# Performance work log

Hardware: AMD Instinct MI355X
Metric: run time of the kernel (lower is better)

Reference implementation:

```python
import jax, jax.numpy as jnp
import numpy as np

B, S, D = 2, 4096, 512
H = 8
W = 512            # local attention window size
HD = D // H        # head dim
NC = S // W        # number of chunks
HALF = W // 2      # symmetric half-window


def setup_inputs() -> dict:
    key = jax.random.key(0)
    ks = jax.random.split(key, 12)
    s = 1.0 / np.sqrt(D)
    return {
        "val": jax.random.normal(ks[0], (B, S, D), jnp.float32),
        "Wq": jax.random.normal(ks[1], (D, D), jnp.float32) * s,
        "bq": jnp.zeros((D,), jnp.float32),
        "Wk": jax.random.normal(ks[2], (D, D), jnp.float32) * s,
        "bk": jnp.zeros((D,), jnp.float32),
        "Wv": jax.random.normal(ks[3], (D, D), jnp.float32) * s,
        "bv": jnp.zeros((D,), jnp.float32),
        "Wo": jax.random.normal(ks[4], (D, D), jnp.float32) * s,
        "bo": jnp.zeros((D,), jnp.float32),
        "gamma": jnp.ones((D,), jnp.float32),
        "beta": jnp.zeros((D,), jnp.float32),
    }


def _heads(x):
    # [B,S,D] -> [B,H,S,HD]
    return x.reshape(B, S, H, HD).transpose(0, 2, 1, 3)


def _gather_neighbors(x):
    # x: [B,H,S,HD] -> [B,H,NC,3W,HD] (prev | cur | next chunk, zero-padded at ends)
    xp = jnp.pad(x, ((0, 0), (0, 0), (W, W), (0, 0)))
    xc = xp.reshape(B, H, NC + 2, W, HD)
    return jnp.concatenate([xc[:, :, :-2], xc[:, :, 1:-1], xc[:, :, 2:]], axis=3)


def _local_attention(x, Wq, bq, Wk, bk, Wv, bv, Wo, bo):
    q = _heads(x @ Wq + bq)
    k = _heads(x @ Wk + bk)
    v = _heads(x @ Wv + bv)

    qc = q.reshape(B, H, NC, W, HD)            # chunked queries
    kn = _gather_neighbors(k)                  # [B,H,NC,3W,HD]
    vn = _gather_neighbors(v)

    scale = 1.0 / np.sqrt(HD)
    scores = jnp.einsum("bhcqd,bhckd->bhcqk", qc, kn) * scale  # [B,H,NC,W,3W]

    # banded mask: key relative position in [-HALF, HALF], and key index in [0,S)
    qi = jnp.arange(W)[:, None]
    kj = jnp.arange(3 * W)[None, :]
    band = jnp.abs(kj - W - qi) <= HALF                          # [W,3W]
    key_pos = (jnp.arange(NC)[:, None, None] - 1) * W + kj[None]  # [NC,1,3W]
    valid = (key_pos >= 0) & (key_pos < S)                       # [NC,1,3W]
    mask = band[None] & valid                                    # [NC,W,3W]

    scores = jnp.where(mask[None, None], scores, jnp.float32(-1e9))
    p = jax.nn.softmax(scores, axis=-1)
    o = jnp.einsum("bhcqk,bhckd->bhcqd", p, vn)                  # [B,H,NC,W,HD]
    o = o.reshape(B, H, S, HD).transpose(0, 2, 1, 3).reshape(B, S, D)
    return o @ Wo + bo


def _layer_norm(x, gamma, beta, eps=1e-5):
    mu = jnp.mean(x, axis=-1, keepdims=True)
    var = jnp.mean(jnp.square(x - mu), axis=-1, keepdims=True)
    return (x - mu) * jax.lax.rsqrt(var + eps) * gamma + beta


def reference(val, Wq, bq, Wk, bk, Wv, bv, Wo, bo, gamma, beta):
    attn_out = _local_attention(val, Wq, bq, Wk, bk, Wv, bv, Wo, bo)
    return _layer_norm(val + attn_out, gamma, beta)
```

## Files before the change

kernel.cpp:

```cpp
#include <hip/hip_runtime.h>
#include <hip/hip_bf16.h>

#define BATCH 2
#define SEQ   4096
#define DIM   512
#define NHEAD 8
#define HDIM  64
#define ROWS  (BATCH*SEQ)

typedef float  fx4   __attribute__((ext_vector_type(4)));
typedef __bf16 bf16x8 __attribute__((ext_vector_type(8)));
typedef unsigned short ushort_t;
typedef unsigned short usx4 __attribute__((ext_vector_type(4)));
typedef unsigned short usx8 __attribute__((ext_vector_type(8)));

static __device__ __forceinline__ float b2f(ushort_t v) {
    union { unsigned int u; float f; } c; c.u = ((unsigned int)v) << 16; return c.f;
}
static __device__ __forceinline__ ushort_t f2b(float f) {
    union { float f; unsigned int u; } c; c.f = f;
    unsigned int u = c.u;
    unsigned int r = (u + 0x7FFFu + ((u >> 16) & 1u)) >> 16;
    return (ushort_t)r;
}
static __device__ __forceinline__ void gload16(const ushort_t* g, ushort_t* l) {
    __builtin_amdgcn_global_load_lds(
        (const __attribute__((address_space(1))) unsigned int*)g,
        (__attribute__((address_space(3))) unsigned int*)l, 16, 0, 0);
}

__global__ __launch_bounds__(256) void cvt_bf16_kernel(const float* __restrict__ x,
                                                       ushort_t* __restrict__ y, int n) {
    int i = (blockIdx.x * 256 + threadIdx.x) * 4;
    if (i < n) {
        fx4 v = *(const fx4*)(x + i);
        usx4 o; o.x = f2b(v.x); o.y = f2b(v.y); o.z = f2b(v.z); o.w = f2b(v.w);
        *(usx4*)(y + i) = o;
    }
}

__global__ __launch_bounds__(256) void transpose4_bf16_kernel(
    const float* __restrict__ W0, const float* __restrict__ W1,
    const float* __restrict__ W2, const float* __restrict__ W3,
    ushort_t* __restrict__ T0, ushort_t* __restrict__ T1,
    ushort_t* __restrict__ T2, ushort_t* __restrict__ T3) {
    const float* W; ushort_t* WT;
    switch (blockIdx.y) {
        case 0: W = W0; WT = T0; break;
        case 1: W = W1; WT = T1; break;
        case 2: W = W2; WT = T2; break;
        default: W = W3; WT = T3; break;
    }
    __shared__ float tile[64][65];
    int r0 = (blockIdx.x & 7) * 64;
    int c0 = (blockIdx.x >> 3) * 64;
    int tid = threadIdx.x;
    for (int idx = tid; idx < 4096; idx += 256) {
        int rr = idx >> 6, cc = idx & 63;
        tile[rr][cc] = W[(c0 + rr) * 512 + (r0 + cc)];
    }
    __syncthreads();
    for (int idx = tid; idx < 4096; idx += 256) {
        int rr = idx >> 6, cc = idx & 63;
        WT[(size_t)(r0 + rr) * 512 + (c0 + cc)] = f2b(tile[cc][rr]);
    }
}

__global__ __launch_bounds__(256) void gemm128_kernel(
    const ushort_t* __restrict__ A,
    const ushort_t* __restrict__ BT0, const ushort_t* __restrict__ BT1, const ushort_t* __restrict__ BT2,
    const float* __restrict__ b0, const float* __restrict__ b1, const float* __restrict__ b2,
    ushort_t* __restrict__ C0, ushort_t* __restrict__ C1, ushort_t* __restrict__ C2) {

    const ushort_t* BT; const float* bias; ushort_t* C;
    if (blockIdx.z == 0)      { BT = BT0; bias = b0; C = C0; }
    else if (blockIdx.z == 1) { BT = BT1; bias = b1; C = C1; }
    else                      { BT = BT2; bias = b2; C = C2; }

    __shared__ ushort_t As[2][128 * 32];
    __shared__ ushort_t Bs[2][128 * 32];

    const int tid  = threadIdx.x;
    const int wave = tid >> 6;
    const int lane = tid & 63;
    const int lm   = lane & 15;
    const int quad = lane >> 4;
    const int wm   = wave >> 1;
    const int wn   = wave & 1;

    const int m0t = blockIdx.x * 128;
    const int n0t = blockIdx.y * 128;

    const int srow = tid >> 2, sgc = tid & 3;
    const ushort_t* ga0 = A  + (size_t)(m0t + srow) * 512 + sgc * 8;
    const ushort_t* ga1 = A  + (size_t)(m0t + srow + 64) * 512 + sgc * 8;
    const ushort_t* gb0 = BT + (size_t)(n0t + srow) * 512 + sgc * 8;
    const ushort_t* gb1 = BT + (size_t)(n0t + srow + 64) * 512 + sgc * 8;

    const int aoff = (wm * 64 + lm) * 32 + quad * 8;
    const int boff = (wn * 64 + lm) * 32 + quad * 8;

    fx4 acc[4][4];
    #pragma unroll
    for (int i = 0; i < 4; ++i)
        #pragma unroll
        for (int j = 0; j < 4; ++j) acc[i][j] = 0;

    for (int k0 = 0; k0 < 512; k0 += 64) {
        __syncthreads();
        #pragma unroll
        for (int p = 0; p < 2; ++p) {
            gload16(ga0 + k0 + p * 32, &As[p][tid * 8]);
            gload16(ga1 + k0 + p * 32, &As[p][(tid + 256) * 8]);
            gload16(gb0 + k0 + p * 32, &Bs[p][tid * 8]);
            gload16(gb1 + k0 + p * 32, &Bs[p][(tid + 256) * 8]);
        }
        __syncthreads();

        #pragma unroll
        for (int p = 0; p < 2; ++p) {
            bf16x8 af[4], bfr[4];
            #pragma unroll
            for (int ms = 0; ms < 4; ++ms) af[ms]  = *(const bf16x8*)&As[p][aoff + ms * 512];
            #pragma unroll
            for (int ns = 0; ns < 4; ++ns) bfr[ns] = *(const bf16x8*)&Bs[p][boff + ns * 512];
            #pragma unroll
            for (int ms = 0; ms < 4; ++ms)
                #pragma unroll
                for (int ns = 0; ns < 4; ++ns)
                    acc[ms][ns] = __builtin_amdgcn_mfma_f32_16x16x32_bf16(af[ms], bfr[ns], acc[ms][ns], 0, 0, 0);
        }
    }

    const int crow0 = m0t + wm * 64 + quad * 4;
    const int ccol0 = n0t + wn * 64 + lm;

    if (blockIdx.z == 2) {
        #pragma unroll
        for (int ns = 0; ns < 4; ++ns) {
            int col = ccol0 + ns * 16;
            int h = col >> 6, d = col & 63;
            float bv = bias[col];
            #pragma unroll
            for (int ms = 0; ms < 4; ++ms) {
                int m = crow0 + ms * 16;
                int bb = m >> 12, s0 = m & 4095;
                usx4 o;
                o.x = f2b(acc[ms][ns][0] + bv); o.y = f2b(acc[ms][ns][1] + bv);
                o.z = f2b(acc[ms][ns][2] + bv); o.w = f2b(acc[ms][ns][3] + bv);
                *(usx4*)(C + (((size_t)(bb * 8 + h) * 64 + d) * 4096 + s0)) = o;
            }
        }
    } else {
        #pragma unroll
        for (int ns = 0; ns < 4; ++ns) {
            int col = ccol0 + ns * 16;
            float bv = bias[col];
            #pragma unroll
            for (int ms = 0; ms < 4; ++ms) {
                #pragma unroll
                for (int r = 0; r < 4; ++r) {
                    C[(size_t)(crow0 + ms * 16 + r) * 512 + col] = f2b(acc[ms][ns][r] + bv);
                }
            }
        }
    }
}

__global__ __launch_bounds__(256) void attn_mfma_kernel(
    const ushort_t* __restrict__ Qb, const ushort_t* __restrict__ Kb,
    const ushort_t* __restrict__ Vt, ushort_t* __restrict__ Ob) {

    __shared__ ushort_t Klds[64 * 64];
    __shared__ ushort_t Vlds[64 * 64];
    __shared__ ushort_t Plds[4 * 32 * 72];

    const int tid  = threadIdx.x;
    const int wave = tid >> 6;
    const int lane = tid & 63;
    const int lm   = lane & 15;
    const int quad = lane >> 4;

    const int bh = blockIdx.y;
    const int b = bh >> 3, h = bh & 7;
    const int q0 = blockIdx.x * 128;
    const int qw = q0 + wave * 32;

    bf16x8 qf[2][2];
    #pragma unroll
    for (int qs = 0; qs < 2; ++qs) {
        const ushort_t* qp = Qb + ((size_t)(b * SEQ + qw + qs * 16 + lm)) * 512 + h * 64 + quad * 8;
        qf[qs][0] = *(const bf16x8*)qp;
        qf[qs][1] = *(const bf16x8*)(qp + 32);
    }

    int koff[2][4], voff[2][4];
    #pragma unroll
    for (int ks = 0; ks < 2; ++ks) {
        #pragma unroll
        for (int tn = 0; tn < 4; ++tn) {
            int key = tn * 16 + lm;
            koff[ks][tn] = key * 64 + (((ks * 4 + quad) ^ (key & 7)) * 8);
            int d = tn * 16 + lm;
            voff[ks][tn] = d * 64 + (((ks * 4 + quad) ^ (d & 7)) * 8);
        }
    }
    ushort_t* Pw = Plds + wave * (32 * 72);
    int pread[2][2];
    #pragma unroll
    for (int qs = 0; qs < 2; ++qs)
        #pragma unroll
        for (int ks = 0; ks < 2; ++ks)
            pread[qs][ks] = (qs * 16 + lm) * 72 + ks * 32 + quad * 8;

    const int skey = tid >> 3;
    const int sdg  = tid & 7;
    const size_t kgbase = ((size_t)b * SEQ) * 512 + h * 64 + sdg * 8;
    const size_t vgbase = ((size_t)bh * 64) * 4096 + sdg * 8;
    const int l0 = skey * 64 + ((sdg ^ (skey & 7)) * 8);
    const int l1 = l0 + 32 * 64;

    const int klo = (q0 >= 256) ? 0 : ((256 - q0) >> 6);
    const int khi = min(9, (4288 - q0) >> 6);
    const int wlo = wave >> 1, whi = 8 + (wave >> 1);
    const int flo = 1 + (wave >> 1), fhi = 7 + (wave >> 1);

    bf16x8 onesf;
    {
        __bf16 o = (lm == 0) ? (__bf16)1.0f : (__bf16)0.0f;
        #pragma unroll
        for (int j = 0; j < 8; ++j) onesf[j] = o;
    }

    fx4 oacc[2][4];
    #pragma unroll
    for (int qs = 0; qs < 2; ++qs)
        #pragma unroll
        for (int tn = 0; tn < 4; ++tn) oacc[qs][tn] = 0;
    fx4 lacc[2];
    lacc[0] = 0; lacc[1] = 0;

    usx8 kn0, kn1, vn0, vn1;
    {
        int ts = q0 - 256 + klo * 64;
        kn0 = *(const usx8*)(Kb + kgbase + (size_t)(ts + skey) * 512);
        kn1 = *(const usx8*)(Kb + kgbase + (size_t)(ts + skey + 32) * 512);
        vn0 = *(const usx8*)(Vt + vgbase + (size_t)skey * 4096 + ts);
        vn1 = *(const usx8*)(Vt + vgbase + (size_t)(skey + 32) * 4096 + ts);
    }

    for (int kt = klo; kt <= khi; ++kt) {
        const int ts = q0 - 256 + kt * 64;
        __syncthreads();
        *(usx8*)&Klds[l0] = kn0;
        *(usx8*)&Klds[l1] = kn1;
        *(usx8*)&Vlds[l0] = vn0;
        *(usx8*)&Vlds[l1] = vn1;
        __syncthreads();

        if (kt < khi) {
            int t2 = ts + 64;
            kn0 = *(const usx8*)(Kb + kgbase + (size_t)(t2 + skey) * 512);
            kn1 = *(const usx8*)(Kb + kgbase + (size_t)(t2 + skey + 32) * 512);
            vn0 = *(const usx8*)(Vt + vgbase + (size_t)skey * 4096 + t2);
            vn1 = *(const usx8*)(Vt + vgbase + (size_t)(skey + 32) * 4096 + t2);
        }

        if (kt < wlo || kt > whi) continue;

        bf16x8 kf[2][4];
        #pragma unroll
        for (int ks = 0; ks < 2; ++ks)
            #pragma unroll
            for (int tn = 0; tn < 4; ++tn)
                kf[ks][tn] = *(const bf16x8*)&Klds[koff[ks][tn]];
        fx4 sacc[2][4];
        #pragma unroll
        for (int qs = 0; qs < 2; ++qs)
            #pragma unroll
            for (int tn = 0; tn < 4; ++tn) sacc[qs][tn] = 0;
        #pragma unroll
        for (int ks = 0; ks < 2; ++ks)
            #pragma unroll
            for (int tn = 0; tn < 4; ++tn) {
                sacc[0][tn] = __builtin_amdgcn_mfma_f32_16x16x32_bf16(qf[0][ks], kf[ks][tn], sacc[0][tn], 0, 0, 0);
                sacc[1][tn] = __builtin_amdgcn_mfma_f32_16x16x32_bf16(qf[1][ks], kf[ks][tn], sacc[1][tn], 0, 0, 0);
            }

        const bool edge = (kt < flo) || (kt > fhi);
        #pragma unroll
        for (int qs = 0; qs < 2; ++qs) {
            #pragma unroll
            for (int tn = 0; tn < 4; ++tn) {
                int kg = ts + tn * 16 + lm;
                #pragma unroll
                for (int r = 0; r < 4; ++r) {
                    float p = __expf(sacc[qs][tn][r] * 0.125f);
                    if (edge) {
                        int dlt = kg - (qw + qs * 16 + quad * 4 + r);
                        p = (dlt <= 256 && dlt >= -256) ? p : 0.0f;
                    }
                    Pw[(qs * 16 + quad * 4 + r) * 72 + tn * 16 + lm] = f2b(p);
                }
            }
        }

        bf16x8 vf[2][4];
        #pragma unroll
        for (int ks = 0; ks < 2; ++ks)
            #pragma unroll
            for (int tn = 0; tn < 4; ++tn)
                vf[ks][tn] = *(const bf16x8*)&Vlds[voff[ks][tn]];
        #pragma unroll
        for (int qs = 0; qs < 2; ++qs) {
            #pragma unroll
            for (int ks = 0; ks < 2; ++ks) {
                bf16x8 ap = *(const bf16x8*)&Pw[pread[qs][ks]];
                lacc[qs] = __builtin_amdgcn_mfma_f32_16x16x32_bf16(ap, onesf, lacc[qs], 0, 0, 0);
                #pragma unroll
                for (int tn = 0; tn < 4; ++tn)
                    oacc[qs][tn] = __builtin_amdgcn_mfma_f32_16x16x32_bf16(ap, vf[ks][tn], oacc[qs][tn], 0, 0, 0);
            }
        }
    }

    #pragma unroll
    for (int qs = 0; qs < 2; ++qs) {
        float linv[4];
        #pragma unroll
        for (int r = 0; r < 4; ++r) {
            float lv = __shfl(lacc[qs][r], (lane & 48));
            linv[r] = 1.0f / lv;
        }
        ushort_t* ob = Ob + ((size_t)(b * SEQ + qw + qs * 16 + quad * 4)) * 512 + h * 64 + lm;
        #pragma unroll
        for (int tn = 0; tn < 4; ++tn)
            #pragma unroll
            for (int r = 0; r < 4; ++r)
                ob[(size_t)r * 512 + tn * 16] = f2b(oacc[qs][tn][r] * linv[r]);
    }
}

__global__ __launch_bounds__(256) void ln_kernel(
    const float* __restrict__ x, const ushort_t* __restrict__ ob,
    const float* __restrict__ gamma, const float* __restrict__ beta,
    float* __restrict__ out) {

    int row  = blockIdx.x * 4 + (threadIdx.x >> 6);
    int lane = threadIdx.x & 63;

    const float*    xp = x  + (size_t)row * 512 + lane * 8;
    const ushort_t* op = ob + (size_t)row * 512 + lane * 8;

    fx4 xa = ((const fx4*)xp)[0];
    fx4 xb = ((const fx4*)xp)[1];
    usx4 oa = ((const usx4*)op)[0];
    usx4 oc = ((const usx4*)op)[1];
    fx4 va, vb;
    va.x = xa.x + b2f(oa.x); va.y = xa.y + b2f(oa.y); va.z = xa.z + b2f(oa.z); va.w = xa.w + b2f(oa.w);
    vb.x = xb.x + b2f(oc.x); vb.y = xb.y + b2f(oc.y); vb.z = xb.z + b2f(oc.z); vb.w = xb.w + b2f(oc.w);

    float s = va.x + va.y + va.z + va.w + vb.x + vb.y + vb.z + vb.w;
    #pragma unroll
    for (int m = 32; m > 0; m >>= 1) s += __shfl_xor(s, m);
    float mu = s * (1.0f / 512.0f);

    fx4 da = va - mu;
    fx4 db = vb - mu;
    float ss = da.x*da.x + da.y*da.y + da.z*da.z + da.w*da.w
             + db.x*db.x + db.y*db.y + db.z*db.z + db.w*db.w;
    #pragma unroll
    for (int m = 32; m > 0; m >>= 1) ss += __shfl_xor(ss, m);
    float rstd = rsqrtf(ss * (1.0f / 512.0f) + 1e-5f);

    const fx4* gp = (const fx4*)(gamma + lane * 8);
    const fx4* bp = (const fx4*)(beta  + lane * 8);
    fx4 g0 = gp[0], g1 = gp[1], b0 = bp[0], b1 = bp[1];

    float* outp = out + (size_t)row * 512 + lane * 8;
    fx4 r0 = da * rstd * g0 + b0;
    fx4 r1 = db * rstd * g1 + b1;
    ((fx4*)outp)[0] = r0;
    ((fx4*)outp)[1] = r1;
}

extern "C" void kernel_launch(void* const* d_in, const int* in_sizes, int n_in,
                              void* d_out, int out_size, void* d_ws, size_t ws_size,
                              hipStream_t stream) {
    const float* val   = (const float*)d_in[0];
    const float* Wq    = (const float*)d_in[1];
    const float* bq    = (const float*)d_in[2];
    const float* Wk    = (const float*)d_in[3];
    const float* bk    = (const float*)d_in[4];
    const float* Wv    = (const float*)d_in[5];
    const float* bv    = (const float*)d_in[6];
    const float* Wo    = (const float*)d_in[7];
    const float* bo    = (const float*)d_in[8];
    const float* gamma = (const float*)d_in[9];
    const float* beta  = (const float*)d_in[10];
    float* out = (float*)d_out;

    char* w = (char*)d_ws;
    ushort_t* xb    = (ushort_t*)w; w += (size_t)ROWS * 512 * 2;
    ushort_t* WqT   = (ushort_t*)w; w += 512 * 512 * 2;
    ushort_t* WkT   = (ushort_t*)w; w += 512 * 512 * 2;
    ushort_t* WvT   = (ushort_t*)w; w += 512 * 512 * 2;
    ushort_t* WoT   = (ushort_t*)w; w += 512 * 512 * 2;
    ushort_t* Qb    = (ushort_t*)w; w += (size_t)ROWS * 512 * 2;
    ushort_t* Kb    = (ushort_t*)w; w += (size_t)ROWS * 512 * 2;
    ushort_t* Vtb   = (ushort_t*)w; w += (size_t)ROWS * 512 * 2;
    ushort_t* attnb = (ushort_t*)w; w += (size_t)ROWS * 512 * 2;
    ushort_t* obuf  = (ushort_t*)w; w += (size_t)ROWS * 512 * 2;

    int nelem = ROWS * 512;
    cvt_bf16_kernel<<<nelem / (256 * 4), 256, 0, stream>>>(val, xb, nelem);
    transpose4_bf16_kernel<<<dim3(64, 4), 256, 0, stream>>>(
        Wq, Wk, Wv, Wo, WqT, WkT, WvT, WoT);

    gemm128_kernel<<<dim3(ROWS / 128, 4, 3), 256, 0, stream>>>(
        xb, WqT, WkT, WvT, bq, bk, bv, Qb, Kb, Vtb);

    attn_mfma_kernel<<<dim3(SEQ / 128, BATCH * NHEAD), 256, 0, stream>>>(Qb, Kb, Vtb, attnb);

    gemm128_kernel<<<dim3(ROWS / 128, 4, 1), 256, 0, stream>>>(
        attnb, WoT, WoT, WoT, bo, bo, bo, obuf, obuf, obuf);

    ln_kernel<<<ROWS / 4, 256, 0, stream>>>(val, obuf, gamma, beta, out);
}
```

Baseline: 172.7 us.

## Fuse prep kernels, double-buffer GEMM K loop, read bf16 residual in LayerNorm

After: 182.5 us. 1.06x slower.

```diff
diff --git a/kernel.cpp b/kernel.cpp
--- a/kernel.cpp
+++ b/kernel.cpp
@@ -29,21 +29,23 @@
         (__attribute__((address_space(3))) unsigned int*)l, 16, 0, 0);
 }
 
-__global__ __launch_bounds__(256) void cvt_bf16_kernel(const float* __restrict__ x,
-                                                       ushort_t* __restrict__ y, int n) {
-    int i = (blockIdx.x * 256 + threadIdx.x) * 4;
-    if (i < n) {
-        fx4 v = *(const fx4*)(x + i);
-        usx4 o; o.x = f2b(v.x); o.y = f2b(v.y); o.z = f2b(v.z); o.w = f2b(v.w);
-        *(usx4*)(y + i) = o;
-    }
-}
-
-__global__ __launch_bounds__(256) void transpose4_bf16_kernel(
+__global__ __launch_bounds__(256) void prep_kernel(
+    const float* __restrict__ val, ushort_t* __restrict__ xb,
     const float* __restrict__ W0, const float* __restrict__ W1,
     const float* __restrict__ W2, const float* __restrict__ W3,
     ushort_t* __restrict__ T0, ushort_t* __restrict__ T1,
     ushort_t* __restrict__ T2, ushort_t* __restrict__ T3) {
+
+    const int tid = threadIdx.x;
+    if (blockIdx.y == 4) {
+        const int stride = 64 * 256 * 4;
+        for (int i = (blockIdx.x * 256 + tid) * 4; i < ROWS * 512; i += stride) {
+            fx4 v = *(const fx4*)(val + i);
+            usx4 o; o.x = f2b(v.x); o.y = f2b(v.y); o.z = f2b(v.z); o.w = f2b(v.w);
+            *(usx4*)(xb + i) = o;
+        }
+        return;
+    }
     const float* W; ushort_t* WT;
     switch (blockIdx.y) {
         case 0: W = W0; WT = T0; break;
@@ -54,7 +56,6 @@
     __shared__ float tile[64][65];
     int r0 = (blockIdx.x & 7) * 64;
     int c0 = (blockIdx.x >> 3) * 64;
-    int tid = threadIdx.x;
     for (int idx = tid; idx < 4096; idx += 256) {
         int rr = idx >> 6, cc = idx & 63;
         tile[rr][cc] = W[(c0 + rr) * 512 + (r0 + cc)];
@@ -93,9 +94,9 @@
 
     const int srow = tid >> 2, sgc = tid & 3;
     const ushort_t* ga0 = A  + (size_t)(m0t + srow) * 512 + sgc * 8;
-    const ushort_t* ga1 = A  + (size_t)(m0t + srow + 64) * 512 + sgc * 8;
+    const ushort_t* ga1 = ga0 + (size_t)64 * 512;
     const ushort_t* gb0 = BT + (size_t)(n0t + srow) * 512 + sgc * 8;
-    const ushort_t* gb1 = BT + (size_t)(n0t + srow + 64) * 512 + sgc * 8;
+    const ushort_t* gb1 = gb0 + (size_t)64 * 512;
 
     const int aoff = (wm * 64 + lm) * 32 + quad * 8;
     const int boff = (wn * 64 + lm) * 32 + quad * 8;
@@ -106,30 +107,31 @@
         #pragma unroll
         for (int j = 0; j < 4; ++j) acc[i][j] = 0;
 
-    for (int k0 = 0; k0 < 512; k0 += 64) {
+    gload16(ga0, &As[0][tid * 8]);
+    gload16(ga1, &As[0][(tid + 256) * 8]);
+    gload16(gb0, &Bs[0][tid * 8]);
+    gload16(gb1, &Bs[0][(tid + 256) * 8]);
+
+    for (int it = 0; it < 16; ++it) {
+        const int cur = it & 1, nxt = cur ^ 1;
         __syncthreads();
-        #pragma unroll
-        for (int p = 0; p < 2; ++p) {
-            gload16(ga0 + k0 + p * 32, &As[p][tid * 8]);
-            gload16(ga1 + k0 + p * 32, &As[p][(tid + 256) * 8]);
-            gload16(gb0 + k0 + p * 32, &Bs[p][tid * 8]);
-            gload16(gb1 + k0 + p * 32, &Bs[p][(tid + 256) * 8]);
-        }
-        __syncthreads();
-
-        #pragma unroll
-        for (int p = 0; p < 2; ++p) {
-            bf16x8 af[4], bfr[4];
-            #pragma unroll
-            for (int ms = 0; ms < 4; ++ms) af[ms]  = *(const bf16x8*)&As[p][aoff + ms * 512];
-            #pragma unroll
-            for (int ns = 0; ns < 4; ++ns) bfr[ns] = *(const bf16x8*)&Bs[p][boff + ns * 512];
-            #pragma unroll
-            for (int ms = 0; ms < 4; ++ms)
-                #pragma unroll
-                for (int ns = 0; ns < 4; ++ns)
-                    acc[ms][ns] = __builtin_amdgcn_mfma_f32_16x16x32_bf16(af[ms], bfr[ns], acc[ms][ns], 0, 0, 0);
-        }
+        if (it < 15) {
+            const int k0 = (it + 1) * 32;
+            gload16(ga0 + k0, &As[nxt][tid * 8]);
+            gload16(ga1 + k0, &As[nxt][(tid + 256) * 8]);
+            gload16(gb0 + k0, &Bs[nxt][tid * 8]);
+            gload16(gb1 + k0, &Bs[nxt][(tid + 256) * 8]);
+        }
+        bf16x8 af[4], bfr[4];
+        #pragma unroll
+        for (int ms = 0; ms < 4; ++ms) af[ms]  = *(const bf16x8*)&As[cur][aoff + ms * 512];
+        #pragma unroll
+        for (int ns = 0; ns < 4; ++ns) bfr[ns] = *(const bf16x8*)&Bs[cur][boff + ns * 512];
+        #pragma unroll
+        for (int ms = 0; ms < 4; ++ms)
+            #pragma unroll
+            for (int ns = 0; ns < 4; ++ns)
+                acc[ms][ns] = __builtin_amdgcn_mfma_f32_16x16x32_bf16(af[ms], bfr[ns], acc[ms][ns], 0, 0, 0);
     }
 
     const int crow0 = m0t + wm * 64 + quad * 4;
@@ -342,23 +344,25 @@
 }
 
 __global__ __launch_bounds__(256) void ln_kernel(
-    const float* __restrict__ x, const ushort_t* __restrict__ ob,
+    const ushort_t* __restrict__ xb, const ushort_t* __restrict__ ob,
     const float* __restrict__ gamma, const float* __restrict__ beta,
     float* __restrict__ out) {
 
     int row  = blockIdx.x * 4 + (threadIdx.x >> 6);
     int lane = threadIdx.x & 63;
 
-    const float*    xp = x  + (size_t)row * 512 + lane * 8;
+    const ushort_t* xp = xb + (size_t)row * 512 + lane * 8;
     const ushort_t* op = ob + (size_t)row * 512 + lane * 8;
 
-    fx4 xa = ((const fx4*)xp)[0];
-    fx4 xb = ((const fx4*)xp)[1];
+    usx4 xa = ((const usx4*)xp)[0];
+    usx4 xc = ((const usx4*)xp)[1];
     usx4 oa = ((const usx4*)op)[0];
     usx4 oc = ((const usx4*)op)[1];
     fx4 va, vb;
-    va.x = xa.x + b2f(oa.x); va.y = xa.y + b2f(oa.y); va.z = xa.z + b2f(oa.z); va.w = xa.w + b2f(oa.w);
-    vb.x = xb.x + b2f(oc.x); vb.y = xb.y + b2f(oc.y); vb.z = xb.z + b2f(oc.z); vb.w = xb.w + b2f(oc.w);
+    va.x = b2f(xa.x) + b2f(oa.x); va.y = b2f(xa.y) + b2f(oa.y);
+    va.z = b2f(xa.z) + b2f(oa.z); va.w = b2f(xa.w) + b2f(oa.w);
+    vb.x = b2f(xc.x) + b2f(oc.x); vb.y = b2f(xc.y) + b2f(oc.y);
+    vb.z = b2f(xc.z) + b2f(oc.z); vb.w = b2f(xc.w) + b2f(oc.w);
 
     float s = va.x + va.y + va.z + va.w + vb.x + vb.y + vb.z + vb.w;
     #pragma unroll
@@ -412,10 +416,8 @@
     ushort_t* attnb = (ushort_t*)w; w += (size_t)ROWS * 512 * 2;
     ushort_t* obuf  = (ushort_t*)w; w += (size_t)ROWS * 512 * 2;
 
-    int nelem = ROWS * 512;
-    cvt_bf16_kernel<<<nelem / (256 * 4), 256, 0, stream>>>(val, xb, nelem);
-    transpose4_bf16_kernel<<<dim3(64, 4), 256, 0, stream>>>(
-        Wq, Wk, Wv, Wo, WqT, WkT, WvT, WoT);
+    prep_kernel<<<dim3(64, 5), 256, 0, stream>>>(
+        val, xb, Wq, Wk, Wv, Wo, WqT, WkT, WvT, WoT);
 
     gemm128_kernel<<<dim3(ROWS / 128, 4, 3), 256, 0, stream>>>(
         xb, WqT, WkT, WvT, bq, bk, bv, Qb, Kb, Vtb);
@@ -425,5 +427,5 @@
     gemm128_kernel<<<dim3(ROWS / 128, 4, 1), 256, 0, stream>>>(
         attnb, WoT, WoT, WoT, bo, bo, bo, obuf, obuf, obuf);
 
-    ln_kernel<<<ROWS / 4, 256, 0, stream>>>(val, obuf, gamma, beta, out);
-}
+    ln_kernel<<<ROWS / 4, 256, 0, stream>>>(xb, obuf, gamma, beta, out);
+}
```
